# Optimization experiments

Hardware: AMD Instinct MI355X
Metric: run time of the kernel (lower is better)

Reference implementation:

```python
import jax, jax.numpy as jnp
import numpy as np

EMBED_DIM = 1280
NUM_HEADS = 16
PROJ_SIZE = 1280
HEAD_DIM = PROJ_SIZE // NUM_HEADS  # 80
ROT_HALF = HEAD_DIM // 2           # 40
SEQ = 2048
BS = 1


def setup_inputs() -> dict:
    key = jax.random.key(0)
    ks = jax.random.split(key, 6)
    x = jax.random.normal(ks[0], (SEQ, BS, EMBED_DIM), dtype=jnp.float32)
    rotary_pos_emb = jax.random.normal(ks[1], (SEQ, ROT_HALF), dtype=jnp.float32)
    # four equal-length image segments
    cu_seqlens = jnp.array([0, 512, 1024, 1536, 2048], dtype=jnp.int32)
    qkv_w = jax.random.normal(ks[2], (3 * PROJ_SIZE, EMBED_DIM), dtype=jnp.float32) * (EMBED_DIM ** -0.5)
    qkv_b = jnp.zeros((3 * PROJ_SIZE,), dtype=jnp.float32)
    proj_w = jax.random.normal(ks[3], (EMBED_DIM, PROJ_SIZE), dtype=jnp.float32) * (PROJ_SIZE ** -0.5)
    proj_b = jnp.zeros((EMBED_DIM,), dtype=jnp.float32)
    return {"x": x, "rotary_pos_emb": rotary_pos_emb, "cu_seqlens": cu_seqlens,
            "max_seqlen": 512, "qkv_w": qkv_w, "qkv_b": qkv_b,
            "proj_w": proj_w, "proj_b": proj_b}


def _apply_rotary(t, cos, sin):
    # t: [b, s, h, d]; cos/sin: [s, r] with rotary dim = 2r (here 2r == d)
    r = cos.shape[-1]
    cos = cos[None, :, None, :]
    sin = sin[None, :, None, :]
    t1, t2, rest = t[..., :r], t[..., r:2 * r], t[..., 2 * r:]
    rot = jnp.concatenate([t1 * cos - t2 * sin, t2 * cos + t1 * sin], axis=-1)
    return jnp.concatenate([rot, rest], axis=-1) if rest.shape[-1] else rot


def reference(x, rotary_pos_emb, cu_seqlens, max_seqlen, qkv_w, qkv_b, proj_w, proj_b):
    s, b, _ = x.shape
    qkv = x @ qkv_w.T + qkv_b                      # [s, b, 3*H*D]
    q, k, v = jnp.split(qkv, 3, axis=2)
    # [s, b, H, D] -> [b, s, H, D]
    q, k, v = (t.reshape(s, b, NUM_HEADS, HEAD_DIM).transpose(1, 0, 2, 3) for t in (q, k, v))
    cos, sin = jnp.cos(rotary_pos_emb), jnp.sin(rotary_pos_emb)
    q = _apply_rotary(q, cos, sin)
    k = _apply_rotary(k, cos, sin)
    # varlen attention: tokens attend only within their cu_seqlens segment
    pos = jnp.arange(s)
    seg = jnp.searchsorted(cu_seqlens[1:], pos, side='right')  # [s]
    mask = seg[:, None] == seg[None, :]                        # [s, s]
    scale = HEAD_DIM ** -0.5
    scores = jnp.einsum('bshd,bthd->bhst', q, k) * scale       # [b, H, s, s]
    scores = jnp.where(mask[None, None], scores, jnp.finfo(scores.dtype).min)
    probs = jax.nn.softmax(scores, axis=-1)
    out = jnp.einsum('bhst,bthd->bshd', probs, v)              # [b, s, H, D]
    ctx = out.transpose(1, 0, 2, 3).reshape(s, b, PROJ_SIZE)   # [s, b, H*D]
    return ctx @ proj_w.T + proj_b                             # [s, b, embed_dim]
```

## Files before the change

### kernel.cpp

```cpp
#include <hip/hip_runtime.h>
#include <hip/hip_bf16.h>
#include <cstdint>
#include <cstddef>

#define EMBED 1280
#define NHEAD 16
#define HD 80
#define ROT 40
#define SEQL 2048
#define QKV_N 3840
#define QKV_STRIDE (NHEAD * SEQL * HD)

typedef __attribute__((ext_vector_type(8))) short short8v;
typedef __attribute__((ext_vector_type(4))) short short4v;
typedef __attribute__((ext_vector_type(4))) float f32x4;

__device__ inline unsigned short f2bf(float f) {
    unsigned u = __float_as_uint(f);
    u += 0x7FFFu + ((u >> 16) & 1u);
    return (unsigned short)(u >> 16);
}
__device__ inline float bf2f(unsigned short h) {
    return __uint_as_float(((unsigned)h) << 16);
}

#define GLD16(GP, LP)                                                         \
    __builtin_amdgcn_global_load_lds(                                         \
        (const __attribute__((address_space(1))) unsigned int*)(GP),          \
        (__attribute__((address_space(3))) unsigned int*)(LP), 16, 0, 0)

__global__ __launch_bounds__(256) void split3_kernel(
    const float* __restrict__ s0, unsigned short* __restrict__ h0, unsigned short* __restrict__ l0, int c0,
    const float* __restrict__ s1, unsigned short* __restrict__ h1, unsigned short* __restrict__ l1, int c1,
    const float* __restrict__ s2, unsigned short* __restrict__ h2, unsigned short* __restrict__ l2, int c2)
{
    int i = blockIdx.x * 256 + threadIdx.x;
    const float* s; unsigned short *hp, *lp; int base;
    if (i < c0)               { s = s0; hp = h0; lp = l0; base = i; }
    else if (i < c0 + c1)     { s = s1; hp = h1; lp = l1; base = i - c0; }
    else if (i < c0 + c1 + c2){ s = s2; hp = h2; lp = l2; base = i - c0 - c1; }
    else return;
    float4 v = reinterpret_cast<const float4*>(s)[base];
    unsigned short a0 = f2bf(v.x), a1 = f2bf(v.y), a2 = f2bf(v.z), a3 = f2bf(v.w);
    short4v hv, lv;
    hv[0] = (short)a0; hv[1] = (short)a1; hv[2] = (short)a2; hv[3] = (short)a3;
    lv[0] = (short)f2bf(v.x - bf2f(a0));
    lv[1] = (short)f2bf(v.y - bf2f(a1));
    lv[2] = (short)f2bf(v.z - bf2f(a2));
    lv[3] = (short)f2bf(v.w - bf2f(a3));
    *reinterpret_cast<short4v*>(&hp[base * 4]) = hv;
    *reinterpret_cast<short4v*>(&lp[base * 4]) = lv;
}

template <int MODE>
__global__ __launch_bounds__(256) void gemm_mfma_kernel(
    const float* __restrict__ A, const float* __restrict__ B,
    const float* __restrict__ bias, float* __restrict__ C,
    int M, int N, int K)
{
    __shared__ unsigned short As[2 * 128 * 32];
    __shared__ unsigned short Bs[2 * 128 * 32];

    const int tid  = threadIdx.x;
    const int m0   = blockIdx.y * 128;
    const int n0   = blockIdx.x * 128;
    const int wave = tid >> 6;
    const int lane = tid & 63;
    const int wm   = (wave >> 1) * 64;
    const int wn   = (wave & 1) * 64;
    const int lrow = lane & 15;
    const int lg   = lane >> 4;

    f32x4 acc[4][4];
#pragma unroll
    for (int i = 0; i < 4; ++i)
#pragma unroll
        for (int j = 0; j < 4; ++j) acc[i][j] = (f32x4){0.f, 0.f, 0.f, 0.f};

    for (int k0 = 0; k0 < K; k0 += 32) {
        float4 ar[4], br[4];
#pragma unroll
        for (int l = 0; l < 4; ++l) {
            int id = l * 256 + tid;
            int r = id >> 3, c = id & 7;
            ar[l] = *reinterpret_cast<const float4*>(&A[(size_t)(m0 + r) * K + k0 + c * 4]);
            br[l] = *reinterpret_cast<const float4*>(&B[(size_t)(n0 + r) * K + k0 + c * 4]);
        }
        __syncthreads();
#pragma unroll
        for (int l = 0; l < 4; ++l) {
            int id = l * 256 + tid;
            int r = id >> 3, c = id & 7;
            int base = r * 32 + (((c >> 1) ^ (r & 3)) << 3) + ((c & 1) << 2);
            float4 v = ar[l];
            unsigned short h0 = f2bf(v.x), h1 = f2bf(v.y), h2 = f2bf(v.z), h3 = f2bf(v.w);
            unsigned short g0 = f2bf(v.x - bf2f(h0)), g1 = f2bf(v.y - bf2f(h1));
            unsigned short g2 = f2bf(v.z - bf2f(h2)), g3 = f2bf(v.w - bf2f(h3));
            uint2 w;
            w.x = (unsigned)h0 | ((unsigned)h1 << 16); w.y = (unsigned)h2 | ((unsigned)h3 << 16);
            *reinterpret_cast<uint2*>(&As[base]) = w;
            w.x = (unsigned)g0 | ((unsigned)g1 << 16); w.y = (unsigned)g2 | ((unsigned)g3 << 16);
            *reinterpret_cast<uint2*>(&As[4096 + base]) = w;
            v = br[l];
            h0 = f2bf(v.x); h1 = f2bf(v.y); h2 = f2bf(v.z); h3 = f2bf(v.w);
            g0 = f2bf(v.x - bf2f(h0)); g1 = f2bf(v.y - bf2f(h1));
            g2 = f2bf(v.z - bf2f(h2)); g3 = f2bf(v.w - bf2f(h3));
            w.x = (unsigned)h0 | ((unsigned)h1 << 16); w.y = (unsigned)h2 | ((unsigned)h3 << 16);
            *reinterpret_cast<uint2*>(&Bs[base]) = w;
            w.x = (unsigned)g0 | ((unsigned)g1 << 16); w.y = (unsigned)g2 | ((unsigned)g3 << 16);
            *reinterpret_cast<uint2*>(&Bs[4096 + base]) = w;
        }
        __syncthreads();
        short8v bh[4], bl[4];
#pragma unroll
        for (int fn = 0; fn < 4; ++fn) {
            int row = wn + fn * 16 + lrow;
            int idx = row * 32 + ((lg ^ (row & 3)) << 3);
            bh[fn] = *reinterpret_cast<const short8v*>(&Bs[idx]);
            bl[fn] = *reinterpret_cast<const short8v*>(&Bs[4096 + idx]);
        }
#pragma unroll
        for (int fm = 0; fm < 4; ++fm) {
            int row = wm + fm * 16 + lrow;
            int idx = row * 32 + ((lg ^ (row & 3)) << 3);
            short8v ah = *reinterpret_cast<const short8v*>(&As[idx]);
            short8v al = *reinterpret_cast<const short8v*>(&As[4096 + idx]);
#pragma unroll
            for (int fn = 0; fn < 4; ++fn) {
                acc[fm][fn] = __builtin_amdgcn_mfma_f32_16x16x32_bf16(ah, bh[fn], acc[fm][fn], 0, 0, 0);
                acc[fm][fn] = __builtin_amdgcn_mfma_f32_16x16x32_bf16(ah, bl[fn], acc[fm][fn], 0, 0, 0);
                acc[fm][fn] = __builtin_amdgcn_mfma_f32_16x16x32_bf16(al, bh[fn], acc[fm][fn], 0, 0, 0);
            }
        }
    }

#pragma unroll
    for (int fn = 0; fn < 4; ++fn) {
        int n = n0 + wn + fn * 16 + lrow;
        float bcol = bias[n];
        if (MODE == 0) {
#pragma unroll
            for (int fm = 0; fm < 4; ++fm) {
#pragma unroll
                for (int q = 0; q < 4; ++q) {
                    int m = m0 + wm + fm * 16 + lg * 4 + q;
                    C[(size_t)m * N + n] = acc[fm][fn][q] + bcol;
                }
            }
        } else {
            int part = n / EMBED;
            int rem  = n - part * EMBED;
            int head = rem / HD;
            int d    = rem - head * HD;
            float* dst = C + (size_t)part * QKV_STRIDE + (size_t)head * SEQL * HD + d;
#pragma unroll
            for (int fm = 0; fm < 4; ++fm) {
#pragma unroll
                for (int q = 0; q < 4; ++q) {
                    int m = m0 + wm + fm * 16 + lg * 4 + q;
                    dst[(size_t)m * HD] = acc[fm][fn][q] + bcol;
                }
            }
        }
    }
}

template <int MODE>
__global__ __launch_bounds__(256) void gemm_mfma_pre_kernel(
    const unsigned short* __restrict__ Ah, const unsigned short* __restrict__ Al,
    const unsigned short* __restrict__ Bh, const unsigned short* __restrict__ Bl,
    const float* __restrict__ bias, float* __restrict__ C,
    int M, int N, int K)
{
    __shared__ unsigned short As[2][2 * 128 * 32];
    __shared__ unsigned short Bs[2][2 * 128 * 32];

    const int tid  = threadIdx.x;
    const int m0   = blockIdx.y * 128;
    const int n0   = blockIdx.x * 128;
    const int wave = tid >> 6;
    const int lane = tid & 63;
    const int wm   = (wave >> 1) * 64;
    const int wn   = (wave & 1) * 64;
    const int lrow = lane & 15;
    const int lg   = lane >> 4;

    f32x4 acc[4][4];
#pragma unroll
    for (int i = 0; i < 4; ++i)
#pragma unroll
        for (int j = 0; j < 4; ++j) acc[i][j] = (f32x4){0.f, 0.f, 0.f, 0.f};

    const int r0s = tid >> 2;
    const int r1s = (256 + tid) >> 2;
    const int b0  = tid & 3;
    const int bs0 = b0 ^ (r0s & 3);
    const int bs1 = b0 ^ (r1s & 3);
    const size_t ga0 = (size_t)(m0 + r0s) * K + bs0 * 8;
    const size_t ga1 = (size_t)(m0 + r1s) * K + bs1 * 8;
    const size_t gb0 = (size_t)(n0 + r0s) * K + bs0 * 8;
    const size_t gb1 = (size_t)(n0 + r1s) * K + bs1 * 8;
    const int lo0 = (tid & ~63) * 8;
    const int lo1 = (256 + (tid & ~63)) * 8;

    GLD16(Ah + ga0, &As[0][lo0]);
    GLD16(Ah + ga1, &As[0][lo1]);
    GLD16(Al + ga0, &As[0][lo0 + 4096]);
    GLD16(Al + ga1, &As[0][lo1 + 4096]);
    GLD16(Bh + gb0, &Bs[0][lo0]);
    GLD16(Bh + gb1, &Bs[0][lo1]);
    GLD16(Bl + gb0, &Bs[0][lo0 + 4096]);
    GLD16(Bl + gb1, &Bs[0][lo1 + 4096]);
    __syncthreads();

    const int NT = K >> 5;
    for (int t = 0; t < NT; ++t) {
        const int cur = t & 1, nxt = cur ^ 1;
        if (t + 1 < NT) {
            const size_t k1 = (size_t)(t + 1) * 32;
            GLD16(Ah + ga0 + k1, &As[nxt][lo0]);
            GLD16(Ah + ga1 + k1, &As[nxt][lo1]);
            GLD16(Al + ga0 + k1, &As[nxt][lo0 + 4096]);
            GLD16(Al + ga1 + k1, &As[nxt][lo1 + 4096]);
            GLD16(Bh + gb0 + k1, &Bs[nxt][lo0]);
            GLD16(Bh + gb1 + k1, &Bs[nxt][lo1]);
            GLD16(Bl + gb0 + k1, &Bs[nxt][lo0 + 4096]);
            GLD16(Bl + gb1 + k1, &Bs[nxt][lo1 + 4096]);
        }
        short8v bh[4], bl[4];
#pragma unroll
        for (int fn = 0; fn < 4; ++fn) {
            int row = wn + fn * 16 + lrow;
            int idx = row * 32 + ((lg ^ (row & 3)) << 3);
            bh[fn] = *reinterpret_cast<const short8v*>(&Bs[cur][idx]);
            bl[fn] = *reinterpret_cast<const short8v*>(&Bs[cur][4096 + idx]);
        }
#pragma unroll
        for (int fm = 0; fm < 4; ++fm) {
            int row = wm + fm * 16 + lrow;
            int idx = row * 32 + ((lg ^ (row & 3)) << 3);
            short8v ah = *reinterpret_cast<const short8v*>(&As[cur][idx]);
            short8v al = *reinterpret_cast<const short8v*>(&As[cur][4096 + idx]);
#pragma unroll
            for (int fn = 0; fn < 4; ++fn) {
                acc[fm][fn] = __builtin_amdgcn_mfma_f32_16x16x32_bf16(ah, bh[fn], acc[fm][fn], 0, 0, 0);
                acc[fm][fn] = __builtin_amdgcn_mfma_f32_16x16x32_bf16(ah, bl[fn], acc[fm][fn], 0, 0, 0);
                acc[fm][fn] = __builtin_amdgcn_mfma_f32_16x16x32_bf16(al, bh[fn], acc[fm][fn], 0, 0, 0);
            }
        }
        __syncthreads();
    }

#pragma unroll
    for (int fn = 0; fn < 4; ++fn) {
        int n = n0 + wn + fn * 16 + lrow;
        float bcol = bias[n];
        if (MODE == 0) {
#pragma unroll
            for (int fm = 0; fm < 4; ++fm) {
#pragma unroll
                for (int q = 0; q < 4; ++q) {
                    int m = m0 + wm + fm * 16 + lg * 4 + q;
                    C[(size_t)m * N + n] = acc[fm][fn][q] + bcol;
                }
            }
        } else {
            int part = n / EMBED;
            int rem  = n - part * EMBED;
            int head = rem / HD;
            int d    = rem - head * HD;
            float* dst = C + (size_t)part * QKV_STRIDE + (size_t)head * SEQL * HD + d;
#pragma unroll
            for (int fm = 0; fm < 4; ++fm) {
#pragma unroll
                for (int q = 0; q < 4; ++q) {
                    int m = m0 + wm + fm * 16 + lg * 4 + q;
                    dst[(size_t)m * HD] = acc[fm][fn][q] + bcol;
                }
            }
        }
    }
}

__global__ __launch_bounds__(256) void rotary_kernel(
    float* __restrict__ Q, float* __restrict__ K, const float* __restrict__ rpe)
{
    int idx = blockIdx.x * 256 + threadIdx.x;
    int r = idx % ROT;
    int s = (idx / ROT) & (SEQL - 1);
    int h = (idx / (ROT * SEQL)) & (NHEAD - 1);
    float* buf = (idx >= NHEAD * SEQL * ROT) ? K : Q;
    float* p = buf + ((size_t)h * SEQL + s) * HD;
    float ang = rpe[s * ROT + r];
    float c = cosf(ang), sn = sinf(ang);
    float t1 = p[r], t2 = p[r + ROT];
    p[r]       = t1 * c - t2 * sn;
    p[r + ROT] = t2 * c + t1 * sn;
}

#define KSTR 104
#define VSTR 72
#define PSTR 72

template <int PLANES>
__global__ __launch_bounds__(256) void attn_mfma_kernel(
    const float* __restrict__ Qb, const float* __restrict__ Kb,
    const float* __restrict__ Vb, const int* __restrict__ cu, int nseg,
    float* __restrict__ ctx, unsigned short* __restrict__ ctxh,
    unsigned short* __restrict__ ctxl)
{
    __shared__ unsigned short kv_hi[64 * KSTR];
    __shared__ unsigned short kv_lo[64 * KSTR];
    __shared__ unsigned short p_hi[64 * PSTR];
    __shared__ unsigned short p_lo[64 * PSTR];

    const int tid  = threadIdx.x;
    const int lane = tid & 63;
    const int wave = tid >> 6;
    const int lg   = lane >> 4;
    const int col  = lane & 15;
    const int h    = blockIdx.y;
    const int r0   = blockIdx.x * 64;
    const int wrow = wave * 16;

    int qstart[4], qend[4];
#pragma unroll
    for (int q = 0; q < 4; ++q) {
        int row = r0 + wrow + lg * 4 + q;
        int sid = 0;
        for (int i = 1; i <= nseg; ++i) sid += (cu[i] <= row);
        qstart[q] = (sid == 0) ? 0 : cu[sid];
        qend[q]   = (sid >= nseg) ? SEQL : cu[sid + 1];
    }
    int blo, bhi;
    {
        int sid = 0;
        for (int i = 1; i <= nseg; ++i) sid += (cu[i] <= r0);
        blo = (sid == 0) ? 0 : cu[sid];
        sid = 0;
        for (int i = 1; i <= nseg; ++i) sid += (cu[i] <= r0 + 63);
        bhi = (sid >= nseg) ? SEQL : cu[sid + 1];
    }

    const float scale = 0.11180339887498949f;
    short8v qh[3], qlo[3];
    {
        const float* Qr = Qb + ((size_t)h * SEQL + r0 + wrow + col) * HD;
#pragma unroll
        for (int kc = 0; kc < 3; ++kc) {
            int d0 = kc * 32 + lg * 8;
            float v[8];
            if (d0 < HD) {
                float4 f0 = *reinterpret_cast<const float4*>(&Qr[d0]);
                float4 f1 = *reinterpret_cast<const float4*>(&Qr[d0 + 4]);
                v[0] = f0.x * scale; v[1] = f0.y * scale; v[2] = f0.z * scale; v[3] = f0.w * scale;
                v[4] = f1.x * scale; v[5] = f1.y * scale; v[6] = f1.z * scale; v[7] = f1.w * scale;
            } else {
#pragma unroll
                for (int j = 0; j < 8; ++j) v[j] = 0.f;
            }
            short8v hh, ll;
#pragma unroll
            for (int j = 0; j < 8; ++j) {
                unsigned short hb = f2bf(v[j]);
                hh[j] = (short)hb;
                ll[j] = (short)f2bf(v[j] - bf2f(hb));
            }
            qh[kc] = hh; qlo[kc] = ll;
        }
    }

    f32x4 oacc[5];
#pragma unroll
    for (int fn = 0; fn < 5; ++fn) oacc[fn] = (f32x4){0.f, 0.f, 0.f, 0.f};
    float mrun[4] = {-1e30f, -1e30f, -1e30f, -1e30f};
    float lrun[4] = {0.f, 0.f, 0.f, 0.f};

    const float* Kh = Kb + (size_t)h * SEQL * HD;
    const float* Vh = Vb + (size_t)h * SEQL * HD;

    for (int kb = (blo & ~63); kb < bhi; kb += 64) {
        __syncthreads();

        const float* Kt = Kh + (size_t)kb * HD;
#pragma unroll
        for (int l = 0; l < 5; ++l) {
            int idx = tid + l * 256;
            int ky = idx / 20, fc = idx % 20;
            float4 f = *reinterpret_cast<const float4*>(&Kt[ky * HD + fc * 4]);
            int base = ky * KSTR + fc * 4;
            unsigned short h0 = f2bf(f.x), h1 = f2bf(f.y), h2 = f2bf(f.z), h3 = f2bf(f.w);
            uint2 w;
            w.x = (unsigned)h0 | ((unsigned)h1 << 16); w.y = (unsigned)h2 | ((unsigned)h3 << 16);
            *reinterpret_cast<uint2*>(&kv_hi[base]) = w;
            h0 = f2bf(f.x - bf2f(h0)); h1 = f2bf(f.y - bf2f(h1));
            h2 = f2bf(f.z - bf2f(h2)); h3 = f2bf(f.w - bf2f(h3));
            w.x = (unsigned)h0 | ((unsigned)h1 << 16); w.y = (unsigned)h2 | ((unsigned)h3 << 16);
            *reinterpret_cast<uint2*>(&kv_lo[base]) = w;
        }
        {
            int ky = tid >> 2, off = (tid & 3) << 2;
            uint2 z; z.x = 0u; z.y = 0u;
            *reinterpret_cast<uint2*>(&kv_hi[ky * KSTR + 80 + off]) = z;
            *reinterpret_cast<uint2*>(&kv_lo[ky * KSTR + 80 + off]) = z;
        }
        __syncthreads();

        f32x4 sfr[4];
#pragma unroll
        for (int kt = 0; kt < 4; ++kt) {
            f32x4 s = (f32x4){0.f, 0.f, 0.f, 0.f};
#pragma unroll
            for (int kc = 0; kc < 3; ++kc) {
                int bidx = (kt * 16 + col) * KSTR + kc * 32 + lg * 8;
                short8v kh = *reinterpret_cast<const short8v*>(&kv_hi[bidx]);
                short8v kl = *reinterpret_cast<const short8v*>(&kv_lo[bidx]);
                s = __builtin_amdgcn_mfma_f32_16x16x32_bf16(qh[kc],  kh, s, 0, 0, 0);
                s = __builtin_amdgcn_mfma_f32_16x16x32_bf16(qlo[kc], kh, s, 0, 0, 0);
                s = __builtin_amdgcn_mfma_f32_16x16x32_bf16(qh[kc],  kl, s, 0, 0, 0);
            }
            sfr[kt] = s;
        }
        __syncthreads();

        const float* Vt = Vh + (size_t)kb * HD;
        float4 vreg[5];
#pragma unroll
        for (int l = 0; l < 5; ++l) {
            int idx = tid + l * 256;
            int fc = idx >> 6, ky = idx & 63;
            vreg[l] = *reinterpret_cast<const float4*>(&Vt[ky * HD + fc * 4]);
        }

#pragma unroll
        for (int q = 0; q < 4; ++q) {
            float sv[4];
            float mx = -1e30f;
#pragma unroll
            for (int kt = 0; kt < 4; ++kt) {
                int key = kb + kt * 16 + col;
                bool ok = (key >= qstart[q]) && (key < qend[q]);
                sv[kt] = ok ? sfr[kt][q] : -1e30f;
                mx = fmaxf(mx, sv[kt]);
            }
            mx = fmaxf(mx, __shfl_xor(mx, 1));
            mx = fmaxf(mx, __shfl_xor(mx, 2));
            mx = fmaxf(mx, __shfl_xor(mx, 4));
            mx = fmaxf(mx, __shfl_xor(mx, 8));
            float mnew  = fmaxf(mrun[q], mx);
            float alpha = __expf(mrun[q] - mnew);
            float ps = 0.f;
            int prow = (wrow + lg * 4 + q) * PSTR;
#pragma unroll
            for (int kt = 0; kt < 4; ++kt) {
                float p = (sv[kt] > -1e29f) ? __expf(sv[kt] - mnew) : 0.f;
                ps += p;
                unsigned short ph = f2bf(p);
                p_hi[prow + kt * 16 + col] = ph;
                p_lo[prow + kt * 16 + col] = f2bf(p - bf2f(ph));
            }
            ps += __shfl_xor(ps, 1);
            ps += __shfl_xor(ps, 2);
            ps += __shfl_xor(ps, 4);
            ps += __shfl_xor(ps, 8);
            lrun[q] = lrun[q] * alpha + ps;
            mrun[q] = mnew;
#pragma unroll
            for (int fn = 0; fn < 5; ++fn) oacc[fn][q] *= alpha;
        }

#pragma unroll
        for (int l = 0; l < 5; ++l) {
            int idx = tid + l * 256;
            int fc = idx >> 6, ky = idx & 63;
            float4 f = vreg[l];
            float vv[4] = {f.x, f.y, f.z, f.w};
#pragma unroll
            for (int e = 0; e < 4; ++e) {
                unsigned short hb = f2bf(vv[e]);
                kv_hi[(fc * 4 + e) * VSTR + ky] = hb;
                kv_lo[(fc * 4 + e) * VSTR + ky] = f2bf(vv[e] - bf2f(hb));
            }
        }
        __syncthreads();

#pragma unroll
        for (int kc2 = 0; kc2 < 2; ++kc2) {
            int aidx = (wrow + col) * PSTR + kc2 * 32 + lg * 8;
            short8v pah = *reinterpret_cast<const short8v*>(&p_hi[aidx]);
            short8v pal = *reinterpret_cast<const short8v*>(&p_lo[aidx]);
#pragma unroll
            for (int fn = 0; fn < 5; ++fn) {
                int bidx = (fn * 16 + col) * VSTR + kc2 * 32 + lg * 8;
                short8v vh = *reinterpret_cast<const short8v*>(&kv_hi[bidx]);
                short8v vl = *reinterpret_cast<const short8v*>(&kv_lo[bidx]);
                oacc[fn] = __builtin_amdgcn_mfma_f32_16x16x32_bf16(pah, vh, oacc[fn], 0, 0, 0);
                oacc[fn] = __builtin_amdgcn_mfma_f32_16x16x32_bf16(pal, vh, oacc[fn], 0, 0, 0);
                oacc[fn] = __builtin_amdgcn_mfma_f32_16x16x32_bf16(pah, vl, oacc[fn], 0, 0, 0);
            }
        }
    }

#pragma unroll
    for (int q = 0; q < 4; ++q) {
        float inv = 1.f / lrun[q];
        size_t rowoff = (size_t)(r0 + wrow + lg * 4 + q) * EMBED + h * HD;
        if (PLANES) {
#pragma unroll
            for (int fn = 0; fn < 5; ++fn) {
                float val = oacc[fn][q] * inv;
                unsigned short hb = f2bf(val);
                ctxh[rowoff + fn * 16 + col] = hb;
                ctxl[rowoff + fn * 16 + col] = f2bf(val - bf2f(hb));
            }
        } else {
#pragma unroll
            for (int fn = 0; fn < 5; ++fn)
                ctx[rowoff + fn * 16 + col] = oacc[fn][q] * inv;
        }
    }
}

extern "C" void kernel_launch(void* const* d_in, const int* in_sizes, int n_in,
                              void* d_out, int out_size, void* d_ws, size_t ws_size,
                              hipStream_t stream)
{
    const float* x      = (const float*)d_in[0];
    const float* rpe    = (const float*)d_in[1];
    const int*   cu     = (const int*)d_in[2];
    const float* qkv_w  = (const float*)d_in[4];
    const float* qkv_b  = (const float*)d_in[5];
    const float* proj_w = (const float*)d_in[6];
    const float* proj_b = (const float*)d_in[7];

    float* ws  = (float*)d_ws;
    float* Q   = ws;
    float* K   = ws + (size_t)QKV_STRIDE;
    float* V   = ws + (size_t)2 * QKV_STRIDE;
    float* ctx = ws + (size_t)3 * QKV_STRIDE;

    const int nseg = in_sizes[2] - 1;

    const bool HOIST = ws_size >= 68157440ULL;

    if (HOIST) {
        unsigned short* xh   = (unsigned short*)(ws + (size_t)3 * QKV_STRIDE);
        unsigned short* xl   = xh + (size_t)SEQL * EMBED;
        unsigned short* wh   = (unsigned short*)(ws + (size_t)4 * QKV_STRIDE);
        unsigned short* wl   = wh + (size_t)QKV_N * EMBED;
        unsigned short* ctxh = (unsigned short*)(ws + (size_t)4 * QKV_STRIDE);
        unsigned short* ctxl = ctxh + (size_t)SEQL * EMBED;
        unsigned short* ph   = (unsigned short*)((char*)d_ws + 61603840);
        unsigned short* pl   = ph + (size_t)EMBED * EMBED;

        const int c0 = SEQL * EMBED / 4, c1 = QKV_N * EMBED / 4, c2 = EMBED * EMBED / 4;

        split3_kernel<<<(c0 + c1 + c2 + 255) / 256, 256, 0, stream>>>(
            x, xh, xl, c0, qkv_w, wh, wl, c1, proj_w, ph, pl, c2);

        gemm_mfma_pre_kernel<1><<<dim3(QKV_N / 128, SEQL / 128), 256, 0, stream>>>(
            xh, xl, wh, wl, qkv_b, Q, SEQL, QKV_N, EMBED);

        rotary_kernel<<<(2 * NHEAD * SEQL * ROT) / 256, 256, 0, stream>>>(Q, K, rpe);

        attn_mfma_kernel<1><<<dim3(SEQL / 64, NHEAD), 256, 0, stream>>>(
            Q, K, V, cu, nseg, nullptr, ctxh, ctxl);

        gemm_mfma_pre_kernel<0><<<dim3(EMBED / 128, SEQL / 128), 256, 0, stream>>>(
            ctxh, ctxl, ph, pl, proj_b, (float*)d_out, SEQL, EMBED, EMBED);
    } else {
        gemm_mfma_kernel<1><<<dim3(QKV_N / 128, SEQL / 128), 256, 0, stream>>>(
            x, qkv_w, qkv_b, Q, SEQL, QKV_N, EMBED);
        rotary_kernel<<<(2 * NHEAD * SEQL * ROT) / 256, 256, 0, stream>>>(Q, K, rpe);
        attn_mfma_kernel<0><<<dim3(SEQL / 64, NHEAD), 256, 0, stream>>>(
            Q, K, V, cu, nseg, ctx, nullptr, nullptr);
        gemm_mfma_kernel<0><<<dim3(EMBED / 128, SEQL / 128), 256, 0, stream>>>(
            ctx, proj_w, proj_b, (float*)d_out, SEQL, EMBED, EMBED);
    }
}
```

Measured before the change: 275.5 us.

## Pre-split Q/K/V into bf16 hi/lo planes and transpose V for attention

The QKV GEMM epilogue now writes V directly as transposed bf16 hi/lo planes. A new rotary kernel applies rotation and the softmax scale to Q, then emits bf16 hi/lo planes for Q and K. A new attention kernel loads these precomputed planes, so each query block no longer repeats the fp32-to-bf16 split of K/V tiles. This cuts redundant conversion work and global read bytes in attention. The cost is extra plane writes in the producers, strided transposed V stores in the GEMM epilogue, and tighter workspace aliasing.

```diff
diff --git a/kernel.cpp b/kernel.cpp
--- a/kernel.cpp
+++ b/kernel.cpp
@@ -170,6 +170,7 @@
     const unsigned short* __restrict__ Ah, const unsigned short* __restrict__ Al,
     const unsigned short* __restrict__ Bh, const unsigned short* __restrict__ Bl,
     const float* __restrict__ bias, float* __restrict__ C,
+    unsigned short* __restrict__ vth, unsigned short* __restrict__ vtl,
     int M, int N, int K)
 {
     __shared__ unsigned short As[2][2 * 128 * 32];
@@ -269,13 +270,28 @@
             int rem  = n - part * EMBED;
             int head = rem / HD;
             int d    = rem - head * HD;
-            float* dst = C + (size_t)part * QKV_STRIDE + (size_t)head * SEQL * HD + d;
-#pragma unroll
-            for (int fm = 0; fm < 4; ++fm) {
-#pragma unroll
-                for (int q = 0; q < 4; ++q) {
-                    int m = m0 + wm + fm * 16 + lg * 4 + q;
-                    dst[(size_t)m * HD] = acc[fm][fn][q] + bcol;
+            if (part < 2) {
+                float* dst = C + (size_t)part * QKV_STRIDE + (size_t)head * SEQL * HD + d;
+#pragma unroll
+                for (int fm = 0; fm < 4; ++fm) {
+#pragma unroll
+                    for (int q = 0; q < 4; ++q) {
+                        int m = m0 + wm + fm * 16 + lg * 4 + q;
+                        dst[(size_t)m * HD] = acc[fm][fn][q] + bcol;
+                    }
+                }
+            } else {
+                size_t base = ((size_t)head * HD + d) * SEQL;
+#pragma unroll
+                for (int fm = 0; fm < 4; ++fm) {
+#pragma unroll
+                    for (int q = 0; q < 4; ++q) {
+                        int m = m0 + wm + fm * 16 + lg * 4 + q;
+                        float val = acc[fm][fn][q] + bcol;
+                        unsigned short hb = f2bf(val);
+                        vth[base + m] = hb;
+                        vtl[base + m] = f2bf(val - bf2f(hb));
+                    }
                 }
             }
         }
@@ -298,6 +314,34 @@
     p[r + ROT] = t2 * c + t1 * sn;
 }
 
+__global__ __launch_bounds__(256) void rotary_split_kernel(
+    const float* __restrict__ Qf, const float* __restrict__ Kf,
+    const float* __restrict__ rpe,
+    unsigned short* __restrict__ qh, unsigned short* __restrict__ ql,
+    unsigned short* __restrict__ kh, unsigned short* __restrict__ kl)
+{
+    int idx = blockIdx.x * 256 + threadIdx.x;
+    int r = idx % ROT;
+    int s = (idx / ROT) & (SEQL - 1);
+    int h = (idx / (ROT * SEQL)) & (NHEAD - 1);
+    bool isK = idx >= NHEAD * SEQL * ROT;
+    const float* src = isK ? Kf : Qf;
+    unsigned short* oh = isK ? kh : qh;
+    unsigned short* ol = isK ? kl : ql;
+    const float sc = isK ? 1.f : 0.11180339887498949f;
+    const float* p = src + ((size_t)h * SEQL + s) * HD;
+    float ang = rpe[s * ROT + r];
+    float c = cosf(ang), sn = sinf(ang);
+    float t1 = p[r], t2 = p[r + ROT];
+    float a = (t1 * c - t2 * sn) * sc;
+    float b = (t2 * c + t1 * sn) * sc;
+    size_t o = ((size_t)h * SEQL + s) * HD;
+    unsigned short ha = f2bf(a);
+    oh[o + r] = ha;       ol[o + r] = f2bf(a - bf2f(ha));
+    unsigned short hb = f2bf(b);
+    oh[o + r + ROT] = hb; ol[o + r + ROT] = f2bf(b - bf2f(hb));
+}
+
 #define KSTR 104
 #define VSTR 72
 #define PSTR 72
@@ -343,7 +387,7 @@
     }
 
     const float scale = 0.11180339887498949f;
-    short8v qh[3], qlo[3];
+    short8v qhf[3], qlf[3];
     {
         const float* Qr = Qb + ((size_t)h * SEQL + r0 + wrow + col) * HD;
 #pragma unroll
@@ -366,7 +410,7 @@
                 hh[j] = (short)hb;
                 ll[j] = (short)f2bf(v[j] - bf2f(hb));
             }
-            qh[kc] = hh; qlo[kc] = ll;
+            qhf[kc] = hh; qlf[kc] = ll;
         }
     }
 
@@ -381,7 +425,6 @@
 
     for (int kb = (blo & ~63); kb < bhi; kb += 64) {
         __syncthreads();
-
         const float* Kt = Kh + (size_t)kb * HD;
 #pragma unroll
         for (int l = 0; l < 5; ++l) {
@@ -413,11 +456,11 @@
 #pragma unroll
             for (int kc = 0; kc < 3; ++kc) {
                 int bidx = (kt * 16 + col) * KSTR + kc * 32 + lg * 8;
-                short8v kh = *reinterpret_cast<const short8v*>(&kv_hi[bidx]);
-                short8v kl = *reinterpret_cast<const short8v*>(&kv_lo[bidx]);
-                s = __builtin_amdgcn_mfma_f32_16x16x32_bf16(qh[kc],  kh, s, 0, 0, 0);
-                s = __builtin_amdgcn_mfma_f32_16x16x32_bf16(qlo[kc], kh, s, 0, 0, 0);
-                s = __builtin_amdgcn_mfma_f32_16x16x32_bf16(qh[kc],  kl, s, 0, 0, 0);
+                short8v khf = *reinterpret_cast<const short8v*>(&kv_hi[bidx]);
+                short8v klf = *reinterpret_cast<const short8v*>(&kv_lo[bidx]);
+                s = __builtin_amdgcn_mfma_f32_16x16x32_bf16(qhf[kc], khf, s, 0, 0, 0);
+                s = __builtin_amdgcn_mfma_f32_16x16x32_bf16(qlf[kc], khf, s, 0, 0, 0);
+                s = __builtin_amdgcn_mfma_f32_16x16x32_bf16(qhf[kc], klf, s, 0, 0, 0);
             }
             sfr[kt] = s;
         }
@@ -517,6 +560,199 @@
 #pragma unroll
             for (int fn = 0; fn < 5; ++fn)
                 ctx[rowoff + fn * 16 + col] = oacc[fn][q] * inv;
+        }
+    }
+}
+
+__global__ __launch_bounds__(256) void attn_mfma2_kernel(
+    const unsigned short* __restrict__ qh, const unsigned short* __restrict__ ql,
+    const unsigned short* __restrict__ kh, const unsigned short* __restrict__ kl,
+    const unsigned short* __restrict__ vth, const unsigned short* __restrict__ vtl,
+    const int* __restrict__ cu, int nseg,
+    unsigned short* __restrict__ ctxh, unsigned short* __restrict__ ctxl)
+{
+    __shared__ unsigned short kv_hi[64 * KSTR];
+    __shared__ unsigned short kv_lo[64 * KSTR];
+    __shared__ unsigned short p_hi[64 * PSTR];
+    __shared__ unsigned short p_lo[64 * PSTR];
+
+    const int tid  = threadIdx.x;
+    const int lane = tid & 63;
+    const int wave = tid >> 6;
+    const int lg   = lane >> 4;
+    const int col  = lane & 15;
+    const int h    = blockIdx.y;
+    const int r0   = blockIdx.x * 64;
+    const int wrow = wave * 16;
+
+    int qstart[4], qend[4];
+#pragma unroll
+    for (int q = 0; q < 4; ++q) {
+        int row = r0 + wrow + lg * 4 + q;
+        int sid = 0;
+        for (int i = 1; i <= nseg; ++i) sid += (cu[i] <= row);
+        qstart[q] = (sid == 0) ? 0 : cu[sid];
+        qend[q]   = (sid >= nseg) ? SEQL : cu[sid + 1];
+    }
+    int blo, bhi;
+    {
+        int sid = 0;
+        for (int i = 1; i <= nseg; ++i) sid += (cu[i] <= r0);
+        blo = (sid == 0) ? 0 : cu[sid];
+        sid = 0;
+        for (int i = 1; i <= nseg; ++i) sid += (cu[i] <= r0 + 63);
+        bhi = (sid >= nseg) ? SEQL : cu[sid + 1];
+    }
+
+    short8v qfh[3], qfl[3];
+    {
+        const unsigned short* Qh_ = qh + ((size_t)h * SEQL + r0 + wrow + col) * HD;
+        const unsigned short* Ql_ = ql + ((size_t)h * SEQL + r0 + wrow + col) * HD;
+#pragma unroll
+        for (int kc = 0; kc < 3; ++kc) {
+            int d0 = kc * 32 + lg * 8;
+            if (d0 < HD) {
+                qfh[kc] = *reinterpret_cast<const short8v*>(&Qh_[d0]);
+                qfl[kc] = *reinterpret_cast<const short8v*>(&Ql_[d0]);
+            } else {
+                short8v z = {0,0,0,0,0,0,0,0};
+                qfh[kc] = z; qfl[kc] = z;
+            }
+        }
+    }
+
+    f32x4 oacc[5];
+#pragma unroll
+    for (int fn = 0; fn < 5; ++fn) oacc[fn] = (f32x4){0.f, 0.f, 0.f, 0.f};
+    float mrun[4] = {-1e30f, -1e30f, -1e30f, -1e30f};
+    float lrun[4] = {0.f, 0.f, 0.f, 0.f};
+
+    const unsigned short* Khp = kh + (size_t)h * SEQL * HD;
+    const unsigned short* Klp = kl + (size_t)h * SEQL * HD;
+    const unsigned short* Vhp = vth + (size_t)h * HD * SEQL;
+    const unsigned short* Vlp = vtl + (size_t)h * HD * SEQL;
+
+    for (int kb = (blo & ~63); kb < bhi; kb += 64) {
+        __syncthreads();
+
+        const unsigned short* Kth = Khp + (size_t)kb * HD;
+        const unsigned short* Ktl = Klp + (size_t)kb * HD;
+#pragma unroll
+        for (int l = 0; l < 5; ++l) {
+            int idx = tid + l * 256;
+            int ky = idx / 20, fc = idx % 20;
+            *reinterpret_cast<short4v*>(&kv_hi[ky * KSTR + fc * 4]) =
+                *reinterpret_cast<const short4v*>(&Kth[ky * HD + fc * 4]);
+            *reinterpret_cast<short4v*>(&kv_lo[ky * KSTR + fc * 4]) =
+                *reinterpret_cast<const short4v*>(&Ktl[ky * HD + fc * 4]);
+        }
+        {
+            int ky = tid >> 2, off = (tid & 3) << 2;
+            uint2 z; z.x = 0u; z.y = 0u;
+            *reinterpret_cast<uint2*>(&kv_hi[ky * KSTR + 80 + off]) = z;
+            *reinterpret_cast<uint2*>(&kv_lo[ky * KSTR + 80 + off]) = z;
+        }
+        __syncthreads();
+
+        f32x4 sfr[4];
+#pragma unroll
+        for (int kt = 0; kt < 4; ++kt) {
+            f32x4 s = (f32x4){0.f, 0.f, 0.f, 0.f};
+#pragma unroll
+            for (int kc = 0; kc < 3; ++kc) {
+                int bidx = (kt * 16 + col) * KSTR + kc * 32 + lg * 8;
+                short8v khf = *reinterpret_cast<const short8v*>(&kv_hi[bidx]);
+                short8v klf = *reinterpret_cast<const short8v*>(&kv_lo[bidx]);
+                s = __builtin_amdgcn_mfma_f32_16x16x32_bf16(qfh[kc], khf, s, 0, 0, 0);
+                s = __builtin_amdgcn_mfma_f32_16x16x32_bf16(qfl[kc], khf, s, 0, 0, 0);
+                s = __builtin_amdgcn_mfma_f32_16x16x32_bf16(qfh[kc], klf, s, 0, 0, 0);
+            }
+            sfr[kt] = s;
+        }
+        __syncthreads();
+
+        short4v vrh[5], vrl[5];
+#pragma unroll
+        for (int l = 0; l < 5; ++l) {
+            int idx = tid + l * 256;
+            int d = idx >> 4, kg = idx & 15;
+            vrh[l] = *reinterpret_cast<const short4v*>(&Vhp[(size_t)d * SEQL + kb + kg * 4]);
+            vrl[l] = *reinterpret_cast<const short4v*>(&Vlp[(size_t)d * SEQL + kb + kg * 4]);
+        }
+
+#pragma unroll
+        for (int q = 0; q < 4; ++q) {
+            float sv[4];
+            float mx = -1e30f;
+#pragma unroll
+            for (int kt = 0; kt < 4; ++kt) {
+                int key = kb + kt * 16 + col;
+                bool ok = (key >= qstart[q]) && (key < qend[q]);
+                sv[kt] = ok ? sfr[kt][q] : -1e30f;
+                mx = fmaxf(mx, sv[kt]);
+            }
+            mx = fmaxf(mx, __shfl_xor(mx, 1));
+            mx = fmaxf(mx, __shfl_xor(mx, 2));
+            mx = fmaxf(mx, __shfl_xor(mx, 4));
+            mx = fmaxf(mx, __shfl_xor(mx, 8));
+            float mnew  = fmaxf(mrun[q], mx);
+            float alpha = __expf(mrun[q] - mnew);
+            float ps = 0.f;
+            int prow = (wrow + lg * 4 + q) * PSTR;
+#pragma unroll
+            for (int kt = 0; kt < 4; ++kt) {
+                float p = (sv[kt] > -1e29f) ? __expf(sv[kt] - mnew) : 0.f;
+                ps += p;
+                unsigned short ph = f2bf(p);
+                p_hi[prow + kt * 16 + col] = ph;
+                p_lo[prow + kt * 16 + col] = f2bf(p - bf2f(ph));
+            }
+            ps += __shfl_xor(ps, 1);
+            ps += __shfl_xor(ps, 2);
+            ps += __shfl_xor(ps, 4);
+            ps += __shfl_xor(ps, 8);
+            lrun[q] = lrun[q] * alpha + ps;
+            mrun[q] = mnew;
+#pragma unroll
+            for (int fn = 0; fn < 5; ++fn) oacc[fn][q] *= alpha;
+        }
+
+#pragma unroll
+        for (int l = 0; l < 5; ++l) {
+            int idx = tid + l * 256;
+            int d = idx >> 4, kg = idx & 15;
+            *reinterpret_cast<short4v*>(&kv_hi[d * VSTR + kg * 4]) = vrh[l];
+            *reinterpret_cast<short4v*>(&kv_lo[d * VSTR + kg * 4]) = vrl[l];
+        }
+        __syncthreads();
+
+#pragma unroll
+        for (int kc2 = 0; kc2 < 2; ++kc2) {
+            int aidx = (wrow + col) * PSTR + kc2 * 32 + lg * 8;
+            short8v pah = *reinterpret_cast<const short8v*>(&p_hi[aidx]);
+            short8v pal = *reinterpret_cast<const short8v*>(&p_lo[aidx]);
+#pragma unroll
+            for (int fn = 0; fn < 5; ++fn) {
+                int bidx = (fn * 16 + col) * VSTR + kc2 * 32 + lg * 8;
+                short8v vh = *reinterpret_cast<const short8v*>(&kv_hi[bidx]);
+                short8v vl = *reinterpret_cast<const short8v*>(&kv_lo[bidx]);
+                oacc[fn] = __builtin_amdgcn_mfma_f32_16x16x32_bf16(pah, vh, oacc[fn], 0, 0, 0);
+                oacc[fn] = __builtin_amdgcn_mfma_f32_16x16x32_bf16(pal, vh, oacc[fn], 0, 0, 0);
+                oacc[fn] = __builtin_amdgcn_mfma_f32_16x16x32_bf16(pah, vl, oacc[fn], 0, 0, 0);
+            }
+        }
+    }
+
+#pragma unroll
+    for (int q = 0; q < 4; ++q) {
+        float inv = 1.f / lrun[q];
+        size_t rowoff = (size_t)(r0 + wrow + lg * 4 + q) * EMBED + h * HD;
+#pragma unroll
+        for (int fn = 0; fn < 5; ++fn) {
+            float val = oacc[fn][q] * inv;
+            unsigned short hb = f2bf(val);
+            ctxh[rowoff + fn * 16 + col] = hb;
+            ctxl[rowoff + fn * 16 + col] = f2bf(val - bf2f(hb));
         }
     }
 }
@@ -533,25 +769,28 @@
     const float* proj_w = (const float*)d_in[6];
     const float* proj_b = (const float*)d_in[7];
 
-    float* ws  = (float*)d_ws;
-    float* Q   = ws;
-    float* K   = ws + (size_t)QKV_STRIDE;
-    float* V   = ws + (size_t)2 * QKV_STRIDE;
-    float* ctx = ws + (size_t)3 * QKV_STRIDE;
-
     const int nseg = in_sizes[2] - 1;
+    char* wsb = (char*)d_ws;
 
     const bool HOIST = ws_size >= 68157440ULL;
 
     if (HOIST) {
-        unsigned short* xh   = (unsigned short*)(ws + (size_t)3 * QKV_STRIDE);
-        unsigned short* xl   = xh + (size_t)SEQL * EMBED;
-        unsigned short* wh   = (unsigned short*)(ws + (size_t)4 * QKV_STRIDE);
-        unsigned short* wl   = wh + (size_t)QKV_N * EMBED;
-        unsigned short* ctxh = (unsigned short*)(ws + (size_t)4 * QKV_STRIDE);
-        unsigned short* ctxl = ctxh + (size_t)SEQL * EMBED;
-        unsigned short* ph   = (unsigned short*)((char*)d_ws + 61603840);
-        unsigned short* pl   = ph + (size_t)EMBED * EMBED;
+        float* Qf = (float*)wsb;
+        float* Kf = (float*)(wsb + 10485760);
+        unsigned short* ctxh = (unsigned short*)wsb;
+        unsigned short* ctxl = (unsigned short*)(wsb + 5242880);
+        unsigned short* vth = (unsigned short*)(wsb + 20971520);
+        unsigned short* vtl = (unsigned short*)(wsb + 26214400);
+        unsigned short* xh = (unsigned short*)(wsb + 31457280);
+        unsigned short* xl = (unsigned short*)(wsb + 36700160);
+        unsigned short* wh = (unsigned short*)(wsb + 41943040);
+        unsigned short* wl = (unsigned short*)(wsb + 51773440);
+        unsigned short* qph = (unsigned short*)(wsb + 31457280);
+        unsigned short* qpl = (unsigned short*)(wsb + 36700160);
+        unsigned short* kph = (unsigned short*)(wsb + 41943040);
+        unsigned short* kpl = (unsigned short*)(wsb + 47185920);
+        unsigned short* ph = (unsigned short*)(wsb + 61603840);
+        unsigned short* pl = (unsigned short*)(wsb + 64880640);
 
         const int c0 = SEQL * EMBED / 4, c1 = QKV_N * EMBED / 4, c2 = EMBED * EMBED / 4;
 
@@ -559,16 +798,23 @@
             x, xh, xl, c0, qkv_w, wh, wl, c1, proj_w, ph, pl, c2);
 
         gemm_mfma_pre_kernel<1><<<dim3(QKV_N / 128, SEQL / 128), 256, 0, stream>>>(
-            xh, xl, wh, wl, qkv_b, Q, SEQL, QKV_N, EMBED);
-
-        rotary_kernel<<<(2 * NHEAD * SEQL * ROT) / 256, 256, 0, stream>>>(Q, K, rpe);
-
-        attn_mfma_kernel<1><<<dim3(SEQL / 64, NHEAD), 256, 0, stream>>>(
-            Q, K, V, cu, nseg, nullptr, ctxh, ctxl);
+            xh, xl, wh, wl, qkv_b, Qf, vth, vtl, SEQL, QKV_N, EMBED);
+
+        rotary_split_kernel<<<(2 * NHEAD * SEQL * ROT) / 256, 256, 0, stream>>>(
+            Qf, Kf, rpe, qph, qpl, kph, kpl);
+
+        attn_mfma2_kernel<<<dim3(SEQL / 64, NHEAD), 256, 0, stream>>>(
+            qph, qpl, kph, kpl, vth, vtl, cu, nseg, ctxh, ctxl);
 
         gemm_mfma_pre_kernel<0><<<dim3(EMBED / 128, SEQL / 128), 256, 0, stream>>>(
-            ctxh, ctxl, ph, pl, proj_b, (float*)d_out, SEQL, EMBED, EMBED);
+            ctxh, ctxl, ph, pl, proj_b, (float*)d_out, nullptr, nullptr,
+            SEQL, EMBED, EMBED);
     } else {
+        float* ws  = (float*)d_ws;
+        float* Q   = ws;
+        float* K   = ws + (size_t)QKV_STRIDE;
+        float* V   = ws + (size_t)2 * QKV_STRIDE;
+        float* ctx = ws + (size_t)3 * QKV_STRIDE;
         gemm_mfma_kernel<1><<<dim3(QKV_N / 128, SEQL / 128), 256, 0, stream>>>(
             x, qkv_w, qkv_b, Q, SEQL, QKV_N, EMBED);
         rotary_kernel<<<(2 * NHEAD * SEQL * ROT) / 256, 256, 0, stream>>>(Q, K, rpe);
```

Measured after the change: 259.2 us. 1.06x faster.
